# Performance work log

Measured on AMD Instinct MI355X. Metric: run time of the kernel, lower is better.

## Reference

```python
import jax, jax.numpy as jnp
import numpy as np

VOCAB, E, HID, T = 100000, 256, 512, 12
H = HID // 2          # per-direction LSTM hidden
B, S = 64, 256
START, STOP = 10, 11  # tag_to_ix['<START>'], tag_to_ix['<STOP>']
NEG = -10000.0


def setup_inputs() -> dict:
    key = jax.random.key(0)
    ks = jax.random.split(key, 16)
    inp = {
        'batch_sentence': jax.random.randint(ks[0], (B, S), 0, VOCAB),
        'sentence_length': S,
        'batch_chars2': jnp.zeros((1,), jnp.int64 if jax.config.jax_enable_x64 else jnp.int32),
        'chars2_length': 1,
        'emb': jax.random.normal(ks[1], (VOCAB, E), jnp.float32),
        # PyTorch LSTM layout: W_ih [4H, in], W_hh [4H, H], gate order i,f,g,o
        'Wih_f': jax.random.normal(ks[2], (4 * H, E), jnp.float32) * 0.05,
        'Whh_f': jax.random.normal(ks[3], (4 * H, H), jnp.float32) * 0.05,
        'bih_f': jnp.zeros((4 * H,), jnp.float32),
        'bhh_f': jnp.zeros((4 * H,), jnp.float32),
        'Wih_b': jax.random.normal(ks[4], (4 * H, E), jnp.float32) * 0.05,
        'Whh_b': jax.random.normal(ks[5], (4 * H, H), jnp.float32) * 0.05,
        'bih_b': jnp.zeros((4 * H,), jnp.float32),
        'bhh_b': jnp.zeros((4 * H,), jnp.float32),
        'Wt': jax.random.normal(ks[6], (T, HID), jnp.float32) * 0.05,
        'bt': jnp.zeros((T,), jnp.float32),
        'transitions': jax.random.normal(ks[7], (T, T), jnp.float32),
        # init_hidden() draws randn hidden state: h0/c0 [2 dirs, B, H]
        'h0': jax.random.normal(ks[8], (2, B, H), jnp.float32),
        'c0': jax.random.normal(ks[9], (2, B, H), jnp.float32),
    }
    return inp


def _lstm(x, h0, c0, Wih, Whh, bih, bhh):
    # x: [S, B, E] -> hs: [S, B, H]
    def step(carry, xt):
        h, c = carry
        g = xt @ Wih.T + h @ Whh.T + (bih + bhh)
        i, f, gg, o = jnp.split(g, 4, axis=-1)
        c = jax.nn.sigmoid(f) * c + jax.nn.sigmoid(i) * jnp.tanh(gg)
        h = jax.nn.sigmoid(o) * jnp.tanh(c)
        return (h, c), h
    _, hs = jax.lax.scan(step, (h0, c0), x)
    return hs


def _viterbi(feats, transitions):
    # feats: [S, T] emissions for one sequence
    init = jnp.full((T,), NEG, feats.dtype).at[START].set(0.0)

    def step(fv, feat):
        scores = fv[None, :] + transitions            # [next_tag, prev_tag]
        new_fv = jnp.max(scores, axis=1) + feat       # best prev per next
        bptr = jnp.argmax(scores, axis=1)
        return new_fv, bptr

    fv, bptrs = jax.lax.scan(step, init, feats)       # bptrs: [S, T]
    term = fv + transitions[STOP]
    term = term.at[STOP].set(NEG).at[START].set(NEG)  # torch code masks these
    last = jnp.argmax(term)
    score = term[last]

    def back(tag, bptr):
        return bptr[tag], tag                          # y_t = tag at time t
    _, path = jax.lax.scan(back, last, bptrs, reverse=True)
    return score, path


def reference(batch_sentence, sentence_length, batch_chars2, chars2_length,
              emb, Wih_f, Whh_f, bih_f, bhh_f, Wih_b, Whh_b, bih_b, bhh_b,
              Wt, bt, transitions, h0, c0):
    # word embeddings (dropout = identity at inference)
    x = emb[batch_sentence].transpose(1, 0, 2)        # [S, B, E]
    hf = _lstm(x, h0[0], c0[0], Wih_f, Whh_f, bih_f, bhh_f)
    hb = _lstm(x[::-1], h0[1], c0[1], Wih_b, Whh_b, bih_b, bhh_b)[::-1]
    out = jnp.concatenate([hf, hb], axis=-1)          # [S, B, HID]
    feats = out @ Wt.T + bt                           # [S, B, T]
    feats = feats.transpose(1, 0, 2)                  # [B, S, T]
    scores, paths = jax.vmap(_viterbi, in_axes=(0, None))(feats, transitions)
    return scores, paths
```

## Files before the change

kernel.cpp:

```cpp
#include <hip/hip_runtime.h>
#include <cstdint>
#include <cstddef>

#define EDIM 256
#define HID  512
#define NTAG 12
#define HDIM 256
#define BB   64
#define SS   256
#define START_TAG 10
#define STOP_TAG  11
#define NEGV (-10000.0f)
#define NWGD 32
#define UPW  8

typedef __attribute__((ext_vector_type(8))) short bf16x8;
typedef __attribute__((ext_vector_type(4))) float f32x4;

__device__ __forceinline__ unsigned short bf16_rne(float x) {
  union { float f; unsigned u; } a; a.f = x;
  return (unsigned short)((a.u + 0x7fffu + ((a.u >> 16) & 1u)) >> 16);
}
__device__ __forceinline__ float bf16_tof(unsigned short h) {
  union { unsigned u; float f; } a; a.u = ((unsigned)h) << 16; return a.f;
}
__device__ __forceinline__ void unpack8(const unsigned* u, bf16x8& hi, bf16x8& lo) {
#pragma unroll
  for (int j = 0; j < 8; ++j) {
    hi[j] = (short)(u[j] & 0xffffu);
    lo[j] = (short)(u[j] >> 16);
  }
}
__device__ __forceinline__ void pack_hilo(const float* xf, bf16x8& hi, bf16x8& lo) {
#pragma unroll
  for (int j = 0; j < 8; ++j) {
    unsigned short hb = bf16_rne(xf[j]);
    hi[j] = (short)hb;
    lo[j] = (short)bf16_rne(xf[j] - bf16_tof(hb));
  }
}

__global__ void k0_gather(const int* __restrict__ sent,
                          const float* __restrict__ emb,
                          unsigned int* __restrict__ xpk) {
  int t = blockIdx.x;
  for (int n = threadIdx.x; n < BB * EDIM; n += 256) {
    int b = n >> 8, k = n & 255;
    int tok = sent[b * SS + t];
    float x = emb[(size_t)tok * EDIM + k];
    unsigned short hb = bf16_rne(x);
    unsigned short lb = bf16_rne(x - bf16_tof(hb));
    xpk[((size_t)t * BB + b) * EDIM + k] = (unsigned)hb | ((unsigned)lb << 16);
  }
}

__global__ void __launch_bounds__(256)
k1_mfma(const unsigned int* __restrict__ xpk,
        const float* __restrict__ WihF, const float* __restrict__ WihB,
        const float* __restrict__ bihF, const float* __restrict__ bhhF,
        const float* __restrict__ bihB, const float* __restrict__ bhhB,
        float* __restrict__ pre) {
  int blk = blockIdx.x;
  int rg = blk & 15, t = (blk >> 4) & 255, d = blk >> 12;
  const float* Wih = d ? WihB : WihF;
  const float* bi  = d ? bihB : bihF;
  const float* bh2 = d ? bhhB : bhhF;
  int tid = threadIdx.x, lane = tid & 63, v = tid >> 6;
  int l15 = lane & 15, l4 = lane >> 4;

  int Rrow = rg * 64 + v * 16 + l15;
  const float* wrow = Wih + (size_t)Rrow * EDIM;
  bf16x8 Ahi[8], Alo[8];
#pragma unroll
  for (int kk = 0; kk < 8; ++kk) {
    float4 f0 = *(const float4*)(wrow + kk * 32 + l4 * 8);
    float4 f1 = *(const float4*)(wrow + kk * 32 + l4 * 8 + 4);
    float xf[8] = {f0.x, f0.y, f0.z, f0.w, f1.x, f1.y, f1.z, f1.w};
    pack_hilo(xf, Ahi[kk], Alo[kk]);
  }
  float b4[4];
#pragma unroll
  for (int r = 0; r < 4; ++r) {
    int Racc = rg * 64 + v * 16 + l4 * 4 + r;
    b4[r] = bi[Racc] + bh2[Racc];
  }
  const unsigned int* xt = xpk + (size_t)t * BB * EDIM;
  size_t obase = ((size_t)d * SS + t) * 1024 * BB;
#pragma unroll
  for (int ct = 0; ct < 4; ++ct) {
    f32x4 acc = {b4[0], b4[1], b4[2], b4[3]};
    int col = ct * 16 + l15;
    const unsigned int* xc = xt + (size_t)col * EDIM;
#pragma unroll
    for (int kk = 0; kk < 8; ++kk) {
      uint4 q0 = *(const uint4*)(xc + kk * 32 + l4 * 8);
      uint4 q1 = *(const uint4*)(xc + kk * 32 + l4 * 8 + 4);
      unsigned u[8] = {q0.x, q0.y, q0.z, q0.w, q1.x, q1.y, q1.z, q1.w};
      bf16x8 bhf, blf;
      unpack8(u, bhf, blf);
      acc = __builtin_amdgcn_mfma_f32_16x16x32_bf16(Ahi[kk], bhf, acc, 0, 0, 0);
      acc = __builtin_amdgcn_mfma_f32_16x16x32_bf16(Ahi[kk], blf, acc, 0, 0, 0);
      acc = __builtin_amdgcn_mfma_f32_16x16x32_bf16(Alo[kk], bhf, acc, 0, 0, 0);
    }
#pragma unroll
    for (int r = 0; r < 4; ++r) {
      int Racc = rg * 64 + v * 16 + l4 * 4 + r;
      pre[obase + (size_t)Racc * BB + col] = acc[r];
    }
  }
}

__global__ void __launch_bounds__(256, 1)
lstm_mfma(const float* __restrict__ WhhF, const float* __restrict__ WhhB,
          const float* __restrict__ h0, const float* __restrict__ c0,
          const float* __restrict__ pre, float* __restrict__ hseq,
          unsigned int* __restrict__ hx, unsigned int* flags) {
  const int bid = blockIdx.x;
  const int d = bid >> 5, w = bid & 31;
  const int tid = threadIdx.x;
  const int lane = tid & 63;
  const int v = tid >> 6;
  const int l15 = lane & 15, l4 = lane >> 4;
  const float* Whh = d ? WhhB : WhhF;

  __shared__ float Cl[32][65];
  __shared__ float cst[UPW][BB];

  bf16x8 Ahi[2][8], Alo[2][8];
#pragma unroll
  for (int rt = 0; rt < 2; ++rt) {
    int i = rt * 16 + l15;
    int R = ((i >> 3) << 8) + w * UPW + (i & 7);
    const float* wrow = Whh + (size_t)R * HDIM;
#pragma unroll
    for (int kk = 0; kk < 8; ++kk) {
      float4 f0 = *(const float4*)(wrow + kk * 32 + l4 * 8);
      float4 f1 = *(const float4*)(wrow + kk * 32 + l4 * 8 + 4);
      float xf[8] = {f0.x, f0.y, f0.z, f0.w, f1.x, f1.y, f1.z, f1.w};
      pack_hilo(xf, Ahi[rt][kk], Alo[rt][kk]);
    }
  }
  for (int n = tid; n < UPW * BB; n += 256) {
    int u = n >> 6, b = n & 63;
    cst[u][b] = c0[((size_t)d * BB + b) * HDIM + (w * UPW + u)];
  }
  __syncthreads();

  const int bcol = v * 16 + l15;
  unsigned int* myfl = flags + d * 128;

  for (int s = 0; s < SS; ++s) {
    const int t = d ? (SS - 1 - s) : s;

    const float* pbase = pre + (((size_t)d * SS + t) * 1024) * BB + bcol;
    f32x4 acc0, acc1;
#pragma unroll
    for (int r = 0; r < 4; ++r) {
      int i0 = l4 * 4 + r;
      int R0 = ((i0 >> 3) << 8) + w * UPW + (i0 & 7);
      acc0[r] = pbase[(size_t)R0 * BB];
      int i1 = 16 + i0;
      int R1 = ((i1 >> 3) << 8) + w * UPW + (i1 & 7);
      acc1[r] = pbase[(size_t)R1 * BB];
    }

    if (s > 0) {
      const unsigned int tgt = (unsigned int)s;
      const unsigned long long* fp = (const unsigned long long*)myfl + lane;
      while (true) {
        unsigned long long fv = __hip_atomic_load(fp, __ATOMIC_RELAXED, __HIP_MEMORY_SCOPE_AGENT);
        int ok = ((unsigned)fv >= tgt) && ((unsigned)(fv >> 32) >= tgt);
        if (__all(ok)) break;
        __builtin_amdgcn_s_sleep(1);
      }
      __builtin_amdgcn_sched_barrier(0);
    }

    if (s == 0) {
      const float* hrow = h0 + ((size_t)d * BB + bcol) * HDIM;
#pragma unroll
      for (int kk = 0; kk < 8; ++kk) {
        float4 f0 = *(const float4*)(hrow + kk * 32 + l4 * 8);
        float4 f1 = *(const float4*)(hrow + kk * 32 + l4 * 8 + 4);
        float xf[8] = {f0.x, f0.y, f0.z, f0.w, f1.x, f1.y, f1.z, f1.w};
        bf16x8 bh, bl;
        pack_hilo(xf, bh, bl);
        acc0 = __builtin_amdgcn_mfma_f32_16x16x32_bf16(Ahi[0][kk], bh, acc0, 0, 0, 0);
        acc0 = __builtin_amdgcn_mfma_f32_16x16x32_bf16(Ahi[0][kk], bl, acc0, 0, 0, 0);
        acc0 = __builtin_amdgcn_mfma_f32_16x16x32_bf16(Alo[0][kk], bh, acc0, 0, 0, 0);
        acc1 = __builtin_amdgcn_mfma_f32_16x16x32_bf16(Ahi[1][kk], bh, acc1, 0, 0, 0);
        acc1 = __builtin_amdgcn_mfma_f32_16x16x32_bf16(Ahi[1][kk], bl, acc1, 0, 0, 0);
        acc1 = __builtin_amdgcn_mfma_f32_16x16x32_bf16(Alo[1][kk], bh, acc1, 0, 0, 0);
      }
    } else {
      const unsigned int* hb_base =
          hx + (((size_t)d * 2 + (s & 1)) * HDIM) * BB + bcol;
#pragma unroll
      for (int kk = 0; kk < 8; ++kk) {
        unsigned u[8];
#pragma unroll
        for (int j = 0; j < 8; ++j)
          u[j] = __hip_atomic_load(hb_base + (size_t)(kk * 32 + l4 * 8 + j) * BB,
                                   __ATOMIC_RELAXED, __HIP_MEMORY_SCOPE_AGENT);
        bf16x8 bh, bl;
        unpack8(u, bh, bl);
        acc0 = __builtin_amdgcn_mfma_f32_16x16x32_bf16(Ahi[0][kk], bh, acc0, 0, 0, 0);
        acc0 = __builtin_amdgcn_mfma_f32_16x16x32_bf16(Ahi[0][kk], bl, acc0, 0, 0, 0);
        acc0 = __builtin_amdgcn_mfma_f32_16x16x32_bf16(Alo[0][kk], bh, acc0, 0, 0, 0);
        acc1 = __builtin_amdgcn_mfma_f32_16x16x32_bf16(Ahi[1][kk], bh, acc1, 0, 0, 0);
        acc1 = __builtin_amdgcn_mfma_f32_16x16x32_bf16(Ahi[1][kk], bl, acc1, 0, 0, 0);
        acc1 = __builtin_amdgcn_mfma_f32_16x16x32_bf16(Alo[1][kk], bh, acc1, 0, 0, 0);
      }
    }

#pragma unroll
    for (int r = 0; r < 4; ++r) {
      Cl[l4 * 4 + r][bcol] = acc0[r];
      Cl[16 + l4 * 4 + r][bcol] = acc1[r];
    }
    __syncthreads();

    {
      const int par = (s + 1) & 1;
      unsigned int* wdst = hx + (((size_t)d * 2 + par) * HDIM) * BB;
      for (int n = tid; n < UPW * BB; n += 256) {
        int u = n >> 6, b = n & 63;
        float iv = Cl[u][b], fv = Cl[8 + u][b];
        float gv = Cl[16 + u][b], ov = Cl[24 + u][b];
        float si = 1.f / (1.f + expf(-iv));
        float sf = 1.f / (1.f + expf(-fv));
        float so = 1.f / (1.f + expf(-ov));
        float cn = sf * cst[u][b] + si * tanhf(gv);
        cst[u][b] = cn;
        float hn = so * tanhf(cn);
        int kg = w * UPW + u;
        hseq[(((size_t)d * SS + t) * HDIM + kg) * BB + b] = hn;
        unsigned short hb = bf16_rne(hn);
        unsigned short lb = bf16_rne(hn - bf16_tof(hb));
        unsigned int pv = (unsigned int)hb | ((unsigned int)lb << 16);
        __hip_atomic_store(wdst + (size_t)kg * BB + b, pv,
                           __ATOMIC_RELAXED, __HIP_MEMORY_SCOPE_AGENT);
      }
    }
    asm volatile("s_waitcnt vmcnt(0)" ::: "memory");
    if (lane == 0)
      __hip_atomic_store(myfl + w * 4 + v, (unsigned int)(s + 1),
                         __ATOMIC_RELAXED, __HIP_MEMORY_SCOPE_AGENT);
  }
}

__global__ void k3_feats(const float* __restrict__ hseq,
                         const float* __restrict__ Wt,
                         const float* __restrict__ bt,
                         float* __restrict__ feats) {
  int t = blockIdx.x, tid = threadIdx.x;
  __shared__ float Wl[NTAG][HID];
  for (int n = tid; n < NTAG * HID; n += 256) Wl[n >> 9][n & 511] = Wt[n];
  __syncthreads();
  int b = tid & 63, tq = tid >> 6;
  float acc[3];
  for (int c = 0; c < 3; ++c) acc[c] = bt[tq * 3 + c];
  const float* hf = hseq + ((size_t)0 * SS + t) * HDIM * BB;
  const float* hb = hseq + ((size_t)1 * SS + t) * HDIM * BB;
  for (int k = 0; k < HDIM; ++k) {
    float h1 = hf[(size_t)k * BB + b];
    float h2 = hb[(size_t)k * BB + b];
#pragma unroll
    for (int c = 0; c < 3; ++c) {
      acc[c] += h1 * Wl[tq * 3 + c][k];
      acc[c] += h2 * Wl[tq * 3 + c][HDIM + k];
    }
  }
  for (int c = 0; c < 3; ++c)
    feats[((size_t)t * BB + b) * NTAG + tq * 3 + c] = acc[c];
}

__global__ void k4_viterbi(const float* __restrict__ feats,
                           const float* __restrict__ trans,
                           float* __restrict__ out) {
  int b = blockIdx.x, lane = threadIdx.x;
  __shared__ float tr[NTAG][NTAG];
  __shared__ float fv[NTAG], fnew[NTAG], term[NTAG];
  __shared__ unsigned char bp[SS][NTAG];
  for (int n = lane; n < NTAG * NTAG; n += 64) tr[n / NTAG][n % NTAG] = trans[n];
  if (lane < NTAG) fv[lane] = (lane == START_TAG) ? 0.f : NEGV;
  __syncthreads();
  for (int s = 0; s < SS; ++s) {
    if (lane < NTAG) {
      float best = fv[0] + tr[lane][0]; int arg = 0;
#pragma unroll
      for (int j = 1; j < NTAG; ++j) {
        float vv = fv[j] + tr[lane][j];
        if (vv > best) { best = vv; arg = j; }
      }
      fnew[lane] = best + feats[((size_t)s * BB + b) * NTAG + lane];
      bp[s][lane] = (unsigned char)arg;
    }
    __syncthreads();
    if (lane < NTAG) fv[lane] = fnew[lane];
    __syncthreads();
  }
  if (lane < NTAG) {
    float vv = fv[lane] + tr[STOP_TAG][lane];
    if (lane == STOP_TAG || lane == START_TAG) vv = NEGV;
    term[lane] = vv;
  }
  __syncthreads();
  if (lane == 0) {
    float best = term[0]; int arg = 0;
    for (int j = 1; j < NTAG; ++j)
      if (term[j] > best) { best = term[j]; arg = j; }
    out[b] = best;
    int cur = arg;
    for (int s = SS - 1; s >= 0; --s) {
      out[64 + (size_t)b * SS + s] = (float)cur;
      cur = bp[s][cur];
    }
  }
}

extern "C" void kernel_launch(void* const* d_in, const int* in_sizes, int n_in,
                              void* d_out, int out_size, void* d_ws, size_t ws_size,
                              hipStream_t stream) {
  (void)in_sizes; (void)n_in; (void)out_size;
  const int*   sent  = (const int*)d_in[0];
  const float* emb   = (const float*)d_in[4];
  const float* WihF  = (const float*)d_in[5];
  const float* WhhF  = (const float*)d_in[6];
  const float* bihF  = (const float*)d_in[7];
  const float* bhhF  = (const float*)d_in[8];
  const float* WihB  = (const float*)d_in[9];
  const float* WhhB  = (const float*)d_in[10];
  const float* bihB  = (const float*)d_in[11];
  const float* bhhB  = (const float*)d_in[12];
  const float* Wt    = (const float*)d_in[13];
  const float* bt    = (const float*)d_in[14];
  const float* trans = (const float*)d_in[15];
  const float* h0    = (const float*)d_in[16];
  const float* c0    = (const float*)d_in[17];
  float* out = (float*)d_out;

  char* ws = (char*)d_ws;
  unsigned int* flags = (unsigned int*)ws;
  float* pre   = (float*)(ws + 1024);
  float* hseq  = (float*)(ws + 1024 + 134217728ull);
  unsigned int* xpk = (unsigned int*)hseq;
  unsigned int* hx = (unsigned int*)(ws + 1024 + 134217728ull + 33554432ull);
  float* feats = (float*)(ws + 1024 + 134217728ull + 33554432ull + 262144ull);
  if (ws_size < 168821760ull) return;

  hipMemsetAsync(flags, 0, 1024, stream);
  k0_gather<<<SS, 256, 0, stream>>>(sent, emb, xpk);
  k1_mfma<<<8192, 256, 0, stream>>>(xpk, WihF, WihB, bihF, bhhF, bihB, bhhB, pre);
  lstm_mfma<<<64, 256, 0, stream>>>(WhhF, WhhB, h0, c0, pre, hseq, hx, flags);
  k3_feats<<<SS, 256, 0, stream>>>(hseq, Wt, bt, feats);
  k4_viterbi<<<BB, 64, 0, stream>>>(feats, trans, out);
}
```

Measured before the change: 1.934 ms.

## Replace step flags with sentinel-valued hidden-state slots in persistent LSTM

Drops the separate per-wave step counters and instead marks each hidden-state slot with an all-ones sentinel. Consumers poll the packed h values themselves until no sentinel remains, over a 4-deep ring of buffers, and producers reset slots two steps ahead. This removes one flag round-trip and the extra wait per step on the serial recurrence. The gate epilogue is remapped so each thread handles two batch columns with 64-bit stores. The risk is that a genuine packed h value equal to 0xFFFFFFFF would stall the poll, and the wider polling loads add memory traffic while spinning.

Result: faster. 1.597 ms (-17.4%).

```diff
diff --git a/kernel.cpp b/kernel.cpp
--- a/kernel.cpp
+++ b/kernel.cpp
@@ -114,13 +114,15 @@
 lstm_mfma(const float* __restrict__ WhhF, const float* __restrict__ WhhB,
           const float* __restrict__ h0, const float* __restrict__ c0,
           const float* __restrict__ pre, float* __restrict__ hseq,
-          unsigned int* __restrict__ hx, unsigned int* flags) {
+          unsigned int* __restrict__ hx) {
   const int bid = blockIdx.x;
   const int d = bid >> 5, w = bid & 31;
   const int tid = threadIdx.x;
   const int lane = tid & 63;
   const int v = tid >> 6;
   const int l15 = lane & 15, l4 = lane >> 4;
+  const int up = tid >> 5;
+  const int b2 = (tid & 31) * 2;
   const float* Whh = d ? WhhB : WhhF;
 
   __shared__ float Cl[32][65];
@@ -140,14 +142,12 @@
       pack_hilo(xf, Ahi[rt][kk], Alo[rt][kk]);
     }
   }
-  for (int n = tid; n < UPW * BB; n += 256) {
-    int u = n >> 6, b = n & 63;
-    cst[u][b] = c0[((size_t)d * BB + b) * HDIM + (w * UPW + u)];
-  }
+  cst[up][b2]     = c0[((size_t)d * BB + b2)     * HDIM + (w * UPW + up)];
+  cst[up][b2 + 1] = c0[((size_t)d * BB + b2 + 1) * HDIM + (w * UPW + up)];
   __syncthreads();
 
   const int bcol = v * 16 + l15;
-  unsigned int* myfl = flags + d * 128;
+  const int kg = w * UPW + up;
 
   for (int s = 0; s < SS; ++s) {
     const int t = d ? (SS - 1 - s) : s;
@@ -164,16 +164,33 @@
       acc1[r] = pbase[(size_t)R1 * BB];
     }
 
+    unsigned uv[64];
     if (s > 0) {
-      const unsigned int tgt = (unsigned int)s;
-      const unsigned long long* fp = (const unsigned long long*)myfl + lane;
+      const unsigned* slot =
+          hx + (((size_t)d * 4 + ((s - 1) & 3)) * HDIM) * BB + bcol;
       while (true) {
-        unsigned long long fv = __hip_atomic_load(fp, __ATOMIC_RELAXED, __HIP_MEMORY_SCOPE_AGENT);
-        int ok = ((unsigned)fv >= tgt) && ((unsigned)(fv >> 32) >= tgt);
-        if (__all(ok)) break;
+        int bad = 0;
+#pragma unroll
+        for (int kk = 0; kk < 8; ++kk)
+#pragma unroll
+          for (int j = 0; j < 8; ++j) {
+            unsigned val = __hip_atomic_load(
+                slot + (size_t)(kk * 32 + l4 * 8 + j) * BB,
+                __ATOMIC_RELAXED, __HIP_MEMORY_SCOPE_AGENT);
+            uv[kk * 8 + j] = val;
+            bad |= (val == 0xFFFFFFFFu);
+          }
+        if (!__any(bad)) break;
         __builtin_amdgcn_s_sleep(1);
       }
       __builtin_amdgcn_sched_barrier(0);
+    }
+
+    {
+      unsigned long long* ra = (unsigned long long*)(
+          hx + (((size_t)d * 4 + ((s + 1) & 3)) * HDIM + kg) * BB + b2);
+      __hip_atomic_store(ra, 0xFFFFFFFFFFFFFFFFull,
+                         __ATOMIC_RELAXED, __HIP_MEMORY_SCOPE_AGENT);
     }
 
     if (s == 0) {
@@ -193,17 +210,10 @@
         acc1 = __builtin_amdgcn_mfma_f32_16x16x32_bf16(Alo[1][kk], bh, acc1, 0, 0, 0);
       }
     } else {
-      const unsigned int* hb_base =
-          hx + (((size_t)d * 2 + (s & 1)) * HDIM) * BB + bcol;
 #pragma unroll
       for (int kk = 0; kk < 8; ++kk) {
-        unsigned u[8];
-#pragma unroll
-        for (int j = 0; j < 8; ++j)
-          u[j] = __hip_atomic_load(hb_base + (size_t)(kk * 32 + l4 * 8 + j) * BB,
-                                   __ATOMIC_RELAXED, __HIP_MEMORY_SCOPE_AGENT);
         bf16x8 bh, bl;
-        unpack8(u, bh, bl);
+        unpack8(&uv[kk * 8], bh, bl);
         acc0 = __builtin_amdgcn_mfma_f32_16x16x32_bf16(Ahi[0][kk], bh, acc0, 0, 0, 0);
         acc0 = __builtin_amdgcn_mfma_f32_16x16x32_bf16(Ahi[0][kk], bl, acc0, 0, 0, 0);
         acc0 = __builtin_amdgcn_mfma_f32_16x16x32_bf16(Alo[0][kk], bh, acc0, 0, 0, 0);
@@ -220,32 +230,33 @@
     }
     __syncthreads();
 
-    {
-      const int par = (s + 1) & 1;
-      unsigned int* wdst = hx + (((size_t)d * 2 + par) * HDIM) * BB;
-      for (int n = tid; n < UPW * BB; n += 256) {
-        int u = n >> 6, b = n & 63;
-        float iv = Cl[u][b], fv = Cl[8 + u][b];
-        float gv = Cl[16 + u][b], ov = Cl[24 + u][b];
-        float si = 1.f / (1.f + expf(-iv));
-        float sf = 1.f / (1.f + expf(-fv));
-        float so = 1.f / (1.f + expf(-ov));
-        float cn = sf * cst[u][b] + si * tanhf(gv);
-        cst[u][b] = cn;
-        float hn = so * tanhf(cn);
-        int kg = w * UPW + u;
-        hseq[(((size_t)d * SS + t) * HDIM + kg) * BB + b] = hn;
-        unsigned short hb = bf16_rne(hn);
-        unsigned short lb = bf16_rne(hn - bf16_tof(hb));
-        unsigned int pv = (unsigned int)hb | ((unsigned int)lb << 16);
-        __hip_atomic_store(wdst + (size_t)kg * BB + b, pv,
-                           __ATOMIC_RELAXED, __HIP_MEMORY_SCOPE_AGENT);
-      }
-    }
+    float hn[2]; unsigned pv[2];
+#pragma unroll
+    for (int e = 0; e < 2; ++e) {
+      int b = b2 + e;
+      float iv = Cl[up][b], fv = Cl[8 + up][b];
+      float gv = Cl[16 + up][b], ov = Cl[24 + up][b];
+      float si = 1.f / (1.f + expf(-iv));
+      float sf = 1.f / (1.f + expf(-fv));
+      float so = 1.f / (1.f + expf(-ov));
+      float cn = sf * cst[up][b] + si * tanhf(gv);
+      cst[up][b] = cn;
+      float h = so * tanhf(cn);
+      hn[e] = h;
+      unsigned short hb = bf16_rne(h);
+      unsigned short lb = bf16_rne(h - bf16_tof(hb));
+      pv[e] = (unsigned)hb | ((unsigned)lb << 16);
+    }
+    *(float2*)&hseq[(((size_t)d * SS + t) * HDIM + kg) * BB + b2] =
+        make_float2(hn[0], hn[1]);
+
     asm volatile("s_waitcnt vmcnt(0)" ::: "memory");
-    if (lane == 0)
-      __hip_atomic_store(myfl + w * 4 + v, (unsigned int)(s + 1),
-                         __ATOMIC_RELAXED, __HIP_MEMORY_SCOPE_AGENT);
+
+    unsigned long long pv64 =
+        (unsigned long long)pv[0] | ((unsigned long long)pv[1] << 32);
+    unsigned long long* pd = (unsigned long long*)(
+        hx + (((size_t)d * 4 + (s & 3)) * HDIM + kg) * BB + b2);
+    __hip_atomic_store(pd, pv64, __ATOMIC_RELAXED, __HIP_MEMORY_SCOPE_AGENT);
   }
 }
 
@@ -341,18 +352,17 @@
   float* out = (float*)d_out;
 
   char* ws = (char*)d_ws;
-  unsigned int* flags = (unsigned int*)ws;
-  float* pre   = (float*)(ws + 1024);
-  float* hseq  = (float*)(ws + 1024 + 134217728ull);
+  unsigned int* hx = (unsigned int*)ws;
+  float* pre   = (float*)(ws + 524288ull);
+  float* hseq  = (float*)(ws + 524288ull + 134217728ull);
   unsigned int* xpk = (unsigned int*)hseq;
-  unsigned int* hx = (unsigned int*)(ws + 1024 + 134217728ull + 33554432ull);
-  float* feats = (float*)(ws + 1024 + 134217728ull + 33554432ull + 262144ull);
-  if (ws_size < 168821760ull) return;
-
-  hipMemsetAsync(flags, 0, 1024, stream);
+  float* feats = (float*)(ws + 524288ull + 134217728ull + 33554432ull);
+  if (ws_size < 169082880ull) return;
+
+  hipMemsetAsync(hx, 0xFF, 524288ull, stream);
   k0_gather<<<SS, 256, 0, stream>>>(sent, emb, xpk);
   k1_mfma<<<8192, 256, 0, stream>>>(xpk, WihF, WihB, bihF, bhhF, bihB, bhhB, pre);
-  lstm_mfma<<<64, 256, 0, stream>>>(WhhF, WhhB, h0, c0, pre, hseq, hx, flags);
+  lstm_mfma<<<64, 256, 0, stream>>>(WhhF, WhhB, h0, c0, pre, hseq, hx);
   k3_feats<<<SS, 256, 0, stream>>>(hseq, Wt, bt, feats);
   k4_viterbi<<<BB, 64, 0, stream>>>(feats, trans, out);
 }
```

## Fuse both LSTM directions per block and sync via sentinel-tagged ring buffers

Applied to the files above, without the earlier changes.

The recurrent kernel now runs 32 blocks, each handling both the forward and backward direction, so the two independent recurrences interleave and hide each other's latency. The separate flag array and spin on counters is replaced by a 4-slot ring of packed h values that are preset to a 0xFFFFFFFF sentinel. Consumers poll the data itself until no sentinel remains, and producers reset the slot two steps ahead. Gate math is done in registers through a cross-lane shuffle instead of LDS plus __syncthreads, and the MFMA chains are split into six independent accumulators to shorten dependency chains. Costs are doubled weight registers per block, half as many CUs in use, and a correctness risk if a real packed value ever equals the sentinel.

After: 2.579 ms. 33.4% more time.

```diff
diff --git a/kernel.cpp b/kernel.cpp
--- a/kernel.cpp
+++ b/kernel.cpp
@@ -11,7 +11,6 @@
 #define START_TAG 10
 #define STOP_TAG  11
 #define NEGV (-10000.0f)
-#define NWGD 32
 #define UPW  8
 
 typedef __attribute__((ext_vector_type(8))) short bf16x8;
@@ -110,142 +109,165 @@
   }
 }
 
+#define MFMA6(HH, HL, bhf, blf)                                               \
+  accA = __builtin_amdgcn_mfma_f32_16x16x32_bf16(HH[0][kk], bhf, accA, 0, 0, 0); \
+  accB = __builtin_amdgcn_mfma_f32_16x16x32_bf16(HH[0][kk], blf, accB, 0, 0, 0); \
+  accC = __builtin_amdgcn_mfma_f32_16x16x32_bf16(HL[0][kk], bhf, accC, 0, 0, 0); \
+  accD = __builtin_amdgcn_mfma_f32_16x16x32_bf16(HH[1][kk], bhf, accD, 0, 0, 0); \
+  accE = __builtin_amdgcn_mfma_f32_16x16x32_bf16(HH[1][kk], blf, accE, 0, 0, 0); \
+  accF = __builtin_amdgcn_mfma_f32_16x16x32_bf16(HL[1][kk], bhf, accF, 0, 0, 0);
+
+#define SEGMENT(DIRC, HhiX, HloX, c2X, ringX, sX)                             \
+  {                                                                           \
+    const int t = (DIRC) ? (SS - 1 - (sX)) : (sX);                            \
+    const float* pbase =                                                      \
+        pre + (((size_t)(DIRC) * SS + t) * 1024) * BB + bcol;                 \
+    f32x4 accA, accB, accC, accD, accE, accF;                                 \
+    _Pragma("unroll")                                                         \
+    for (int r = 0; r < 4; ++r) {                                             \
+      int i0 = l4 * 4 + r;                                                    \
+      int R0 = ((i0 >> 3) << 8) + w * UPW + (i0 & 7);                         \
+      accA[r] = pbase[(size_t)R0 * BB];                                       \
+      int i1 = 16 + i0;                                                       \
+      int R1 = ((i1 >> 3) << 8) + w * UPW + (i1 & 7);                         \
+      accD[r] = pbase[(size_t)R1 * BB];                                       \
+    }                                                                         \
+    accB = (f32x4){0.f, 0.f, 0.f, 0.f}; accC = accB; accE = accB; accF = accB;\
+    unsigned uv[64];                                                          \
+    if ((sX) > 0) {                                                           \
+      const unsigned* slotp =                                                 \
+          (ringX) + (size_t)(((sX) - 1) & 3) * 16384 + bcol;                  \
+      while (true) {                                                          \
+        int bad = 0;                                                          \
+        _Pragma("unroll")                                                     \
+        for (int kk = 0; kk < 8; ++kk)                                        \
+          _Pragma("unroll")                                                   \
+          for (int j = 0; j < 8; ++j) {                                       \
+            unsigned val = __hip_atomic_load(                                 \
+                slotp + (size_t)(kk * 32 + l4 * 8 + j) * BB,                  \
+                __ATOMIC_RELAXED, __HIP_MEMORY_SCOPE_AGENT);                  \
+            uv[kk * 8 + j] = val;                                             \
+            bad |= (val == 0xFFFFFFFFu);                                      \
+          }                                                                   \
+        if (!__any(bad)) break;                                               \
+        __builtin_amdgcn_s_sleep(1);                                          \
+      }                                                                       \
+      __builtin_amdgcn_sched_barrier(0);                                      \
+    }                                                                         \
+    {                                                                         \
+      unsigned* ra = (ringX) + (size_t)(((sX) + 1) & 3) * 16384;              \
+      __hip_atomic_store(ra + (size_t)kg0 * BB + bcol, 0xFFFFFFFFu,           \
+                         __ATOMIC_RELAXED, __HIP_MEMORY_SCOPE_AGENT);         \
+      __hip_atomic_store(ra + (size_t)(kg0 + 1) * BB + bcol, 0xFFFFFFFFu,     \
+                         __ATOMIC_RELAXED, __HIP_MEMORY_SCOPE_AGENT);         \
+    }                                                                         \
+    if ((sX) == 0) {                                                          \
+      const float* hrow = h0 + ((size_t)(DIRC) * BB + bcol) * HDIM;           \
+      _Pragma("unroll")                                                       \
+      for (int kk = 0; kk < 8; ++kk) {                                        \
+        float4 f0 = *(const float4*)(hrow + kk * 32 + l4 * 8);                \
+        float4 f1 = *(const float4*)(hrow + kk * 32 + l4 * 8 + 4);            \
+        float xf[8] = {f0.x, f0.y, f0.z, f0.w, f1.x, f1.y, f1.z, f1.w};       \
+        bf16x8 bhf, blf;                                                      \
+        pack_hilo(xf, bhf, blf);                                              \
+        MFMA6(HhiX, HloX, bhf, blf)                                           \
+      }                                                                       \
+    } else {                                                                  \
+      _Pragma("unroll")                                                       \
+      for (int kk = 0; kk < 8; ++kk) {                                        \
+        bf16x8 bhf, blf;                                                      \
+        unpack8(&uv[kk * 8], bhf, blf);                                       \
+        MFMA6(HhiX, HloX, bhf, blf)                                           \
+      }                                                                       \
+    }                                                                         \
+    f32x4 acc0 = accA + accB + accC;                                          \
+    f32x4 acc1 = accD + accE + accF;                                          \
+    f32x4 r0, r1;                                                             \
+    _Pragma("unroll")                                                         \
+    for (int r = 0; r < 4; ++r) {                                             \
+      r0[r] = __shfl_xor(acc0[r], 32);                                        \
+      r1[r] = __shfl_xor(acc1[r], 32);                                        \
+    }                                                                         \
+    float hn[2]; unsigned pv[2];                                              \
+    _Pragma("unroll")                                                         \
+    for (int e = 0; e < 2; ++e) {                                             \
+      float iv = low ? acc0[e] : r0[2 + e];                                   \
+      float fv = low ? r0[e] : acc0[2 + e];                                   \
+      float gv = low ? acc1[e] : r1[2 + e];                                   \
+      float ov = low ? r1[e] : acc1[2 + e];                                   \
+      float si = 1.f / (1.f + expf(-iv));                                     \
+      float sf = 1.f / (1.f + expf(-fv));                                     \
+      float so = 1.f / (1.f + expf(-ov));                                     \
+      float cn = sf * (c2X)[e] + si * tanhf(gv);                              \
+      (c2X)[e] = cn;                                                          \
+      float hh = so * tanhf(cn);                                              \
+      hn[e] = hh;                                                             \
+      unsigned short hb2 = bf16_rne(hh);                                      \
+      unsigned short lb2 = bf16_rne(hh - bf16_tof(hb2));                      \
+      pv[e] = (unsigned)hb2 | ((unsigned)lb2 << 16);                          \
+    }                                                                         \
+    asm volatile("s_waitcnt vmcnt(0)" ::: "memory");                          \
+    {                                                                         \
+      unsigned* pd = (ringX) + (size_t)((sX) & 3) * 16384;                    \
+      __hip_atomic_store(pd + (size_t)kg0 * BB + bcol, pv[0],                 \
+                         __ATOMIC_RELAXED, __HIP_MEMORY_SCOPE_AGENT);         \
+      __hip_atomic_store(pd + (size_t)(kg0 + 1) * BB + bcol, pv[1],           \
+                         __ATOMIC_RELAXED, __HIP_MEMORY_SCOPE_AGENT);         \
+    }                                                                         \
+    hseq[(((size_t)(DIRC) * SS + t) * HDIM + kg0) * BB + bcol] = hn[0];       \
+    hseq[(((size_t)(DIRC) * SS + t) * HDIM + kg0 + 1) * BB + bcol] = hn[1];   \
+  }
+
 __global__ void __launch_bounds__(256, 1)
-lstm_mfma(const float* __restrict__ WhhF, const float* __restrict__ WhhB,
+lstm_dual(const float* __restrict__ WhhF, const float* __restrict__ WhhB,
           const float* __restrict__ h0, const float* __restrict__ c0,
           const float* __restrict__ pre, float* __restrict__ hseq,
-          unsigned int* __restrict__ hx, unsigned int* flags) {
-  const int bid = blockIdx.x;
-  const int d = bid >> 5, w = bid & 31;
+          unsigned int* __restrict__ hx) {
+  const int w = blockIdx.x;
   const int tid = threadIdx.x;
   const int lane = tid & 63;
   const int v = tid >> 6;
   const int l15 = lane & 15, l4 = lane >> 4;
-  const float* Whh = d ? WhhB : WhhF;
-
-  __shared__ float Cl[32][65];
-  __shared__ float cst[UPW][BB];
-
-  bf16x8 Ahi[2][8], Alo[2][8];
+  const int bcol = v * 16 + l15;
+  const int u2 = ((l4 & 1) << 2) | ((l4 >> 1) << 1);
+  const bool low = (l4 < 2);
+  const int kg0 = w * UPW + u2;
+
+  bf16x8 HhiF[2][8], HloF[2][8], HhiB[2][8], HloB[2][8];
 #pragma unroll
   for (int rt = 0; rt < 2; ++rt) {
     int i = rt * 16 + l15;
     int R = ((i >> 3) << 8) + w * UPW + (i & 7);
-    const float* wrow = Whh + (size_t)R * HDIM;
+    const float* wrF = WhhF + (size_t)R * HDIM;
+    const float* wrB = WhhB + (size_t)R * HDIM;
 #pragma unroll
     for (int kk = 0; kk < 8; ++kk) {
-      float4 f0 = *(const float4*)(wrow + kk * 32 + l4 * 8);
-      float4 f1 = *(const float4*)(wrow + kk * 32 + l4 * 8 + 4);
-      float xf[8] = {f0.x, f0.y, f0.z, f0.w, f1.x, f1.y, f1.z, f1.w};
-      pack_hilo(xf, Ahi[rt][kk], Alo[rt][kk]);
-    }
-  }
-  for (int n = tid; n < UPW * BB; n += 256) {
-    int u = n >> 6, b = n & 63;
-    cst[u][b] = c0[((size_t)d * BB + b) * HDIM + (w * UPW + u)];
-  }
-  __syncthreads();
-
-  const int bcol = v * 16 + l15;
-  unsigned int* myfl = flags + d * 128;
+      {
+        float4 f0 = *(const float4*)(wrF + kk * 32 + l4 * 8);
+        float4 f1 = *(const float4*)(wrF + kk * 32 + l4 * 8 + 4);
+        float xf[8] = {f0.x, f0.y, f0.z, f0.w, f1.x, f1.y, f1.z, f1.w};
+        pack_hilo(xf, HhiF[rt][kk], HloF[rt][kk]);
+      }
+      {
+        float4 f0 = *(const float4*)(wrB + kk * 32 + l4 * 8);
+        float4 f1 = *(const float4*)(wrB + kk * 32 + l4 * 8 + 4);
+        float xf[8] = {f0.x, f0.y, f0.z, f0.w, f1.x, f1.y, f1.z, f1.w};
+        pack_hilo(xf, HhiB[rt][kk], HloB[rt][kk]);
+      }
+    }
+  }
+  float c2F[2], c2B[2];
+  c2F[0] = c0[((size_t)0 * BB + bcol) * HDIM + kg0];
+  c2F[1] = c0[((size_t)0 * BB + bcol) * HDIM + kg0 + 1];
+  c2B[0] = c0[((size_t)1 * BB + bcol) * HDIM + kg0];
+  c2B[1] = c0[((size_t)1 * BB + bcol) * HDIM + kg0 + 1];
+
+  unsigned int* ringF = hx;
+  unsigned int* ringB = hx + 4 * 16384;
 
   for (int s = 0; s < SS; ++s) {
-    const int t = d ? (SS - 1 - s) : s;
-
-    const float* pbase = pre + (((size_t)d * SS + t) * 1024) * BB + bcol;
-    f32x4 acc0, acc1;
-#pragma unroll
-    for (int r = 0; r < 4; ++r) {
-      int i0 = l4 * 4 + r;
-      int R0 = ((i0 >> 3) << 8) + w * UPW + (i0 & 7);
-      acc0[r] = pbase[(size_t)R0 * BB];
-      int i1 = 16 + i0;
-      int R1 = ((i1 >> 3) << 8) + w * UPW + (i1 & 7);
-      acc1[r] = pbase[(size_t)R1 * BB];
-    }
-
-    if (s > 0) {
-      const unsigned int tgt = (unsigned int)s;
-      const unsigned long long* fp = (const unsigned long long*)myfl + lane;
-      while (true) {
-        unsigned long long fv = __hip_atomic_load(fp, __ATOMIC_RELAXED, __HIP_MEMORY_SCOPE_AGENT);
-        int ok = ((unsigned)fv >= tgt) && ((unsigned)(fv >> 32) >= tgt);
-        if (__all(ok)) break;
-        __builtin_amdgcn_s_sleep(1);
-      }
-      __builtin_amdgcn_sched_barrier(0);
-    }
-
-    if (s == 0) {
-      const float* hrow = h0 + ((size_t)d * BB + bcol) * HDIM;
-#pragma unroll
-      for (int kk = 0; kk < 8; ++kk) {
-        float4 f0 = *(const float4*)(hrow + kk * 32 + l4 * 8);
-        float4 f1 = *(const float4*)(hrow + kk * 32 + l4 * 8 + 4);
-        float xf[8] = {f0.x, f0.y, f0.z, f0.w, f1.x, f1.y, f1.z, f1.w};
-        bf16x8 bh, bl;
-        pack_hilo(xf, bh, bl);
-        acc0 = __builtin_amdgcn_mfma_f32_16x16x32_bf16(Ahi[0][kk], bh, acc0, 0, 0, 0);
-        acc0 = __builtin_amdgcn_mfma_f32_16x16x32_bf16(Ahi[0][kk], bl, acc0, 0, 0, 0);
-        acc0 = __builtin_amdgcn_mfma_f32_16x16x32_bf16(Alo[0][kk], bh, acc0, 0, 0, 0);
-        acc1 = __builtin_amdgcn_mfma_f32_16x16x32_bf16(Ahi[1][kk], bh, acc1, 0, 0, 0);
-        acc1 = __builtin_amdgcn_mfma_f32_16x16x32_bf16(Ahi[1][kk], bl, acc1, 0, 0, 0);
-        acc1 = __builtin_amdgcn_mfma_f32_16x16x32_bf16(Alo[1][kk], bh, acc1, 0, 0, 0);
-      }
-    } else {
-      const unsigned int* hb_base =
-          hx + (((size_t)d * 2 + (s & 1)) * HDIM) * BB + bcol;
-#pragma unroll
-      for (int kk = 0; kk < 8; ++kk) {
-        unsigned u[8];
-#pragma unroll
-        for (int j = 0; j < 8; ++j)
-          u[j] = __hip_atomic_load(hb_base + (size_t)(kk * 32 + l4 * 8 + j) * BB,
-                                   __ATOMIC_RELAXED, __HIP_MEMORY_SCOPE_AGENT);
-        bf16x8 bh, bl;
-        unpack8(u, bh, bl);
-        acc0 = __builtin_amdgcn_mfma_f32_16x16x32_bf16(Ahi[0][kk], bh, acc0, 0, 0, 0);
-        acc0 = __builtin_amdgcn_mfma_f32_16x16x32_bf16(Ahi[0][kk], bl, acc0, 0, 0, 0);
-        acc0 = __builtin_amdgcn_mfma_f32_16x16x32_bf16(Alo[0][kk], bh, acc0, 0, 0, 0);
-        acc1 = __builtin_amdgcn_mfma_f32_16x16x32_bf16(Ahi[1][kk], bh, acc1, 0, 0, 0);
-        acc1 = __builtin_amdgcn_mfma_f32_16x16x32_bf16(Ahi[1][kk], bl, acc1, 0, 0, 0);
-        acc1 = __builtin_amdgcn_mfma_f32_16x16x32_bf16(Alo[1][kk], bh, acc1, 0, 0, 0);
-      }
-    }
-
-#pragma unroll
-    for (int r = 0; r < 4; ++r) {
-      Cl[l4 * 4 + r][bcol] = acc0[r];
-      Cl[16 + l4 * 4 + r][bcol] = acc1[r];
-    }
-    __syncthreads();
-
-    {
-      const int par = (s + 1) & 1;
-      unsigned int* wdst = hx + (((size_t)d * 2 + par) * HDIM) * BB;
-      for (int n = tid; n < UPW * BB; n += 256) {
-        int u = n >> 6, b = n & 63;
-        float iv = Cl[u][b], fv = Cl[8 + u][b];
-        float gv = Cl[16 + u][b], ov = Cl[24 + u][b];
-        float si = 1.f / (1.f + expf(-iv));
-        float sf = 1.f / (1.f + expf(-fv));
-        float so = 1.f / (1.f + expf(-ov));
-        float cn = sf * cst[u][b] + si * tanhf(gv);
-        cst[u][b] = cn;
-        float hn = so * tanhf(cn);
-        int kg = w * UPW + u;
-        hseq[(((size_t)d * SS + t) * HDIM + kg) * BB + b] = hn;
-        unsigned short hb = bf16_rne(hn);
-        unsigned short lb = bf16_rne(hn - bf16_tof(hb));
-        unsigned int pv = (unsigned int)hb | ((unsigned int)lb << 16);
-        __hip_atomic_store(wdst + (size_t)kg * BB + b, pv,
-                           __ATOMIC_RELAXED, __HIP_MEMORY_SCOPE_AGENT);
-      }
-    }
-    asm volatile("s_waitcnt vmcnt(0)" ::: "memory");
-    if (lane == 0)
-      __hip_atomic_store(myfl + w * 4 + v, (unsigned int)(s + 1),
-                         __ATOMIC_RELAXED, __HIP_MEMORY_SCOPE_AGENT);
+    SEGMENT(0, HhiF, HloF, c2F, ringF, s)
+    SEGMENT(1, HhiB, HloB, c2B, ringB, s)
   }
 }
 
@@ -341,18 +363,17 @@
   float* out = (float*)d_out;
 
   char* ws = (char*)d_ws;
-  unsigned int* flags = (unsigned int*)ws;
-  float* pre   = (float*)(ws + 1024);
-  float* hseq  = (float*)(ws + 1024 + 134217728ull);
-  unsigned int* xpk = (unsigned int*)hseq;
-  unsigned int* hx = (unsigned int*)(ws + 1024 + 134217728ull + 33554432ull);
-  float* feats = (float*)(ws + 1024 + 134217728ull + 33554432ull + 262144ull);
-  if (ws_size < 168821760ull) return;
-
-  hipMemsetAsync(flags, 0, 1024, stream);
+  unsigned int* hx  = (unsigned int*)ws;
+  float* pre   = (float*)(ws + 524288ull);
+  unsigned int* xpk = (unsigned int*)(ws + 524288ull + 134217728ull);
+  float* hseq  = (float*)(ws + 524288ull + 134217728ull + 16777216ull);
+  float* feats = (float*)(ws + 524288ull + 134217728ull + 16777216ull + 33554432ull);
+  if (ws_size < 185860096ull) return;
+
+  hipMemsetAsync(hx, 0xFF, 524288ull, stream);
   k0_gather<<<SS, 256, 0, stream>>>(sent, emb, xpk);
   k1_mfma<<<8192, 256, 0, stream>>>(xpk, WihF, WihB, bihF, bhhF, bihB, bhhB, pre);
-  lstm_mfma<<<64, 256, 0, stream>>>(WhhF, WhhB, h0, c0, pre, hseq, hx, flags);
+  lstm_dual<<<32, 256, 0, stream>>>(WhhF, WhhB, h0, c0, pre, hseq, hx);
   k3_feats<<<SS, 256, 0, stream>>>(hseq, Wt, bt, feats);
   k4_viterbi<<<BB, 64, 0, stream>>>(feats, trans, out);
 }
```
